# Kernel tuning notes

Hardware: AMD Instinct MI355X
Metric: run time of the kernel (lower is better)

## Reference

```python
import jax, jax.numpy as jnp
import numpy as np

B, T, D = 4, 2048, 1024

def setup_inputs() -> dict:
    key = jax.random.key(0)
    kx, kq, kk, kv = jax.random.split(key, 4)
    return {
        "vector": jax.random.normal(kx, (B, T, D), dtype=jnp.float32),
        # original uses torch.rand -> uniform [0,1)
        "W_queries": jax.random.uniform(kq, (D, D), dtype=jnp.float32),
        "W_keys": jax.random.uniform(kk, (D, D), dtype=jnp.float32),
        "W_values": jax.random.uniform(kv, (D, D), dtype=jnp.float32),
    }

def reference(vector, W_queries, W_keys, W_values):
    b, num_token, d_out = vector.shape
    queries = vector @ W_queries          # [b, t, d]
    keys = vector @ W_keys                # [b, t, d]
    values = vector @ W_values            # [b, t, d]
    # attention_score: [b, q, k]
    scores = jnp.einsum('bqd,bkd->bqk', queries, keys)
    causal_mask = jnp.triu(jnp.ones((num_token, num_token), dtype=bool), k=1)
    scores = jnp.where(causal_mask[None, :, :], -jnp.inf, scores)
    # NOTE: original uses FLOOR division `//` by sqrt(d_k) -- faithful here.
    inv_sqrt_scale = jnp.asarray(np.sqrt(keys.shape[-1]), dtype=scores.dtype)
    weights = jnp.floor(scores / inv_sqrt_scale)
    # NOTE: original applies softmax over dim=1 (the query axis), not dim=-1.
    weights = jax.nn.softmax(weights, axis=1)
    # dropout rate is 0.0 (eval/deterministic): identity
    context = jnp.einsum('bqk,bkd->bqd', weights, values)
    return context
```

## Files before the change

### kernel.cpp

```cpp
#include <hip/hip_runtime.h>
#include <math.h>

typedef _Float16 half4 __attribute__((ext_vector_type(4)));
typedef _Float16 half8 __attribute__((ext_vector_type(8)));
typedef float f32x4 __attribute__((ext_vector_type(4)));

#define GLD16(gptr, lptr)                                                     \
    __builtin_amdgcn_global_load_lds(                                         \
        (const __attribute__((address_space(1))) unsigned int*)(gptr),        \
        (__attribute__((address_space(3))) unsigned int*)(lptr), 16, 0, 0)

#define WAIT_VM(N) asm volatile("s_waitcnt vmcnt(" #N ")" ::: "memory")
#define WAIT_LGKM0() asm volatile("s_waitcnt lgkmcnt(0)" ::: "memory")
#define BARRIER()  __builtin_amdgcn_s_barrier()
#define SCHED_FENCE() __builtin_amdgcn_sched_barrier(0)

namespace {

constexpr int Bb = 4;
constexpr int Tt = 2048;
constexpr int Dd = 1024;
constexpr int BT = Bb * Tt;
constexpr int NCH = 16;

__device__ inline _Float16 f2h(float f) { return (_Float16)f; }

__global__ __launch_bounds__(256) void convert_all_kernel(
    const float* __restrict__ X,  const float* __restrict__ Wq,
    const float* __restrict__ Wk, const float* __restrict__ Wv,
    _Float16* __restrict__ Xhi, _Float16* __restrict__ Xlo,
    _Float16* __restrict__ Wqh, _Float16* __restrict__ Wql,
    _Float16* __restrict__ Wkh, _Float16* __restrict__ Wkl,
    _Float16* __restrict__ WvTh)
{
    __shared__ float tile[64][65];
    const int f = blockIdx.x;
    if (f < 8192) {
        const int idx = f * 1024 + threadIdx.x * 4;
        const float4 v = *(const float4*)(X + idx);
        const float a[4] = {v.x, v.y, v.z, v.w};
        half4 h, l;
#pragma unroll
        for (int i = 0; i < 4; ++i) {
            h[i] = f2h(a[i]);
            l[i] = f2h(a[i] - (float)h[i]);
        }
        *(half4*)(Xhi + idx) = h;
        *(half4*)(Xlo + idx) = l;
    } else if (f < 10240) {
        const int g = f - 8192;
        const int mat = g >> 10;
        const float* W = mat ? Wk : Wq;
        _Float16* Hh = mat ? Wkh : Wqh;
        _Float16* Ll = mat ? Wkl : Wql;
        const int idx = (g & 1023) * 1024 + threadIdx.x * 4;
        const float4 v = *(const float4*)(W + idx);
        const float a[4] = {v.x, v.y, v.z, v.w};
        half4 h, l;
#pragma unroll
        for (int i = 0; i < 4; ++i) {
            h[i] = f2h(a[i]);
            l[i] = f2h(a[i] - (float)h[i]);
        }
        *(half4*)(Hh + idx) = h;
        *(half4*)(Ll + idx) = l;
    } else {
        const int g = f - 10240;
        const int n0 = (g & 15) * 64, k0 = (g >> 4) * 64;
        const int tx = threadIdx.x & 63, ty = threadIdx.x >> 6;
#pragma unroll
        for (int i = 0; i < 16; ++i)
            tile[ty + i * 4][tx] = Wv[(size_t)(k0 + ty + i * 4) * Dd + n0 + tx];
        __syncthreads();
#pragma unroll
        for (int i = 0; i < 16; ++i) {
            const float v = tile[tx][ty + i * 4];
            WvTh[(size_t)(n0 + ty + i * 4) * Dd + k0 + tx] = f2h(v);
        }
    }
}

__global__ __launch_bounds__(256) void gt_kernel(
    const _Float16* __restrict__ Wkh, const _Float16* __restrict__ Wkl,
    const _Float16* __restrict__ Wqh, const _Float16* __restrict__ Wql,
    _Float16* __restrict__ GTh, _Float16* __restrict__ GTl)
{
    __shared__ _Float16 Ahl[2][2][4][512];
    __shared__ _Float16 Bhl[2][2][4][512];

    const int n0 = blockIdx.x * 64;
    const int m0 = blockIdx.y * 64;
    const int tid = threadIdx.x;
    const int w = tid >> 6, lane = tid & 63;
    const int lr = lane & 15, lq = lane >> 4;
    const int wi = (w >> 1) * 2, wj = (w & 1) * 2;

    f32x4 acc[2][2];
#pragma unroll
    for (int i = 0; i < 2; ++i)
#pragma unroll
        for (int j = 0; j < 2; ++j)
#pragma unroll
            for (int c = 0; c < 4; ++c) acc[i][j][c] = 0.f;

    auto stage = [&](int bf, int kk) {
        const int s = w;
        const size_t ar = (size_t)(m0 + s * 16 + lr) * Dd + kk + lq * 8;
        const size_t br = (size_t)(n0 + s * 16 + lr) * Dd + kk + lq * 8;
        GLD16(Wkh + ar, &Ahl[bf][0][s][0]);
        GLD16(Wkl + ar, &Ahl[bf][1][s][0]);
        GLD16(Wqh + br, &Bhl[bf][0][s][0]);
        GLD16(Wql + br, &Bhl[bf][1][s][0]);
    };

    stage(0, 0);
    int ib = 0;
    for (int step = 0; step < 32; ++step, ib ^= 1) {
        if (step < 31) {
            stage(ib ^ 1, (step + 1) << 5);
            WAIT_VM(4);
        } else {
            WAIT_VM(0);
        }
        BARRIER();
        SCHED_FENCE();
        half8 ah[2], al[2], bh[2], bl[2];
#pragma unroll
        for (int i = 0; i < 2; ++i) {
            ah[i] = *(const half8*)&Ahl[ib][0][wi + i][lane * 8];
            al[i] = *(const half8*)&Ahl[ib][1][wi + i][lane * 8];
        }
#pragma unroll
        for (int j = 0; j < 2; ++j) {
            bh[j] = *(const half8*)&Bhl[ib][0][wj + j][lane * 8];
            bl[j] = *(const half8*)&Bhl[ib][1][wj + j][lane * 8];
        }
#pragma unroll
        for (int i = 0; i < 2; ++i)
#pragma unroll
            for (int j = 0; j < 2; ++j) {
                acc[i][j] = __builtin_amdgcn_mfma_f32_16x16x32_f16(ah[i], bh[j], acc[i][j], 0, 0, 0);
                acc[i][j] = __builtin_amdgcn_mfma_f32_16x16x32_f16(ah[i], bl[j], acc[i][j], 0, 0, 0);
                acc[i][j] = __builtin_amdgcn_mfma_f32_16x16x32_f16(al[i], bh[j], acc[i][j], 0, 0, 0);
            }
        BARRIER();
    }

#pragma unroll
    for (int i = 0; i < 2; ++i)
#pragma unroll
        for (int r = 0; r < 4; ++r) {
            const int row = m0 + (wi + i) * 16 + lq * 4 + r;
#pragma unroll
            for (int j = 0; j < 2; ++j) {
                const int col = n0 + (wj + j) * 16 + lr;
                const float v = acc[i][j][r];
                const _Float16 h = f2h(v);
                GTh[(size_t)row * Dd + col] = h;
                GTl[(size_t)row * Dd + col] = f2h(v - (float)h);
            }
        }
}

__global__ __launch_bounds__(512, 4) void tv_kernel(
    const _Float16* __restrict__ Xhi, const _Float16* __restrict__ Xlo,
    const _Float16* __restrict__ GTh, const _Float16* __restrict__ GTl,
    const _Float16* __restrict__ WvTh,
    _Float16* __restrict__ Thi, _Float16* __restrict__ Tlo,
    _Float16* __restrict__ Vt)
{
    __shared__ _Float16 smem[32768];
    auto A_ = [&](int bf, int hl, int s) -> _Float16* {
        return smem + ((bf * 2 + hl) * 8 + s) * 512;
    };
    auto B_ = [&](int bf, int hl, int s) -> _Float16* {
        return smem + 16384 + ((bf * 2 + hl) * 8 + s) * 512;
    };

    const int f   = blockIdx.x;
    const int xcd = f & 7;
    const int c   = (f >> 3) & 31;
    const int p   = f >> 8;
    const int mb  = xcd * 8 + (c & 7);
    const int sub = p * 4 + (c >> 3);
    const int m0 = mb * 128;
    const int n0 = (sub & 7) * 128;

    const int tid = threadIdx.x;
    const int w = tid >> 6, lane = tid & 63;
    const int lr = lane & 15, lq = lane >> 4;
    const int wr = (w >> 1) * 2;
    const int wc = (w & 1) * 4;

    f32x4 acc[2][4];
#pragma unroll
    for (int i = 0; i < 2; ++i)
#pragma unroll
        for (int j = 0; j < 4; ++j)
#pragma unroll
            for (int c2 = 0; c2 < 4; ++c2) acc[i][j][c2] = 0.f;

    if (sub < 8) {
        auto stage = [&](int bf, int kk) {
            const size_t ar = (size_t)(m0 + w * 16 + lr) * Dd + kk + lq * 8;
            const size_t br = (size_t)(n0 + w * 16 + lr) * Dd + kk + lq * 8;
            GLD16(Xhi + ar, A_(bf, 0, w));
            GLD16(Xlo + ar, A_(bf, 1, w));
            GLD16(GTh + br, B_(bf, 0, w));
            GLD16(GTl + br, B_(bf, 1, w));
        };
        stage(0, 0);
        int ib = 0;
        for (int step = 0; step < 32; ++step, ib ^= 1) {
            if (step < 31) {
                stage(ib ^ 1, (step + 1) << 5);
                WAIT_VM(4);
            } else {
                WAIT_VM(0);
            }
            BARRIER();
            SCHED_FENCE();
            half8 ah[2], al[2], bh[4], bl[4];
#pragma unroll
            for (int i = 0; i < 2; ++i) {
                ah[i] = *(const half8*)(A_(ib, 0, wr + i) + lane * 8);
                al[i] = *(const half8*)(A_(ib, 1, wr + i) + lane * 8);
            }
#pragma unroll
            for (int j = 0; j < 4; ++j) {
                bh[j] = *(const half8*)(B_(ib, 0, wc + j) + lane * 8);
                bl[j] = *(const half8*)(B_(ib, 1, wc + j) + lane * 8);
            }
#pragma unroll
            for (int i = 0; i < 2; ++i)
#pragma unroll
                for (int j = 0; j < 4; ++j) {
                    acc[i][j] = __builtin_amdgcn_mfma_f32_16x16x32_f16(ah[i], bh[j], acc[i][j], 0, 0, 0);
                    acc[i][j] = __builtin_amdgcn_mfma_f32_16x16x32_f16(ah[i], bl[j], acc[i][j], 0, 0, 0);
                    acc[i][j] = __builtin_amdgcn_mfma_f32_16x16x32_f16(al[i], bh[j], acc[i][j], 0, 0, 0);
                }
            BARRIER();
        }
#pragma unroll
        for (int i = 0; i < 2; ++i)
#pragma unroll
            for (int r = 0; r < 4; ++r) {
                const int row = m0 + (wr + i) * 16 + lq * 4 + r;
#pragma unroll
                for (int j = 0; j < 4; ++j) {
                    const int col = n0 + (wc + j) * 16 + lr;
                    const float v = acc[i][j][r];
                    const _Float16 h = f2h(v);
                    Thi[(size_t)row * Dd + col] = h;
                    Tlo[(size_t)row * Dd + col] = f2h(v - (float)h);
                }
            }
    } else {
        auto stage = [&](int bf, int kk) {
            GLD16(Xhi + (size_t)(m0 + w * 16 + lr) * Dd + kk + lq * 8, A_(bf, 0, w));
            GLD16(WvTh + (size_t)(n0 + w * 16 + lr) * Dd + kk + lq * 8, B_(bf, 0, w));
        };
        stage(0, 0);
        int ib = 0;
        for (int step = 0; step < 32; ++step, ib ^= 1) {
            if (step < 31) {
                stage(ib ^ 1, (step + 1) << 5);
                WAIT_VM(2);
            } else {
                WAIT_VM(0);
            }
            BARRIER();
            SCHED_FENCE();
            half8 a[2], b2[4];
#pragma unroll
            for (int i = 0; i < 2; ++i) a[i] = *(const half8*)(A_(ib, 0, wr + i) + lane * 8);
#pragma unroll
            for (int j = 0; j < 4; ++j) b2[j] = *(const half8*)(B_(ib, 0, wc + j) + lane * 8);
#pragma unroll
            for (int i = 0; i < 2; ++i)
#pragma unroll
                for (int j = 0; j < 4; ++j)
                    acc[i][j] = __builtin_amdgcn_mfma_f32_16x16x32_f16(a[i], b2[j], acc[i][j], 0, 0, 0);
            BARRIER();
        }
        __syncthreads();
#pragma unroll
        for (int i = 0; i < 2; ++i)
#pragma unroll
            for (int r2 = 0; r2 < 4; ++r2) {
                const int rloc = (wr + i) * 16 + lq * 4 + r2;
#pragma unroll
                for (int j = 0; j < 4; ++j) {
                    const int cloc = (wc + j) * 16 + lr;
                    smem[cloc * 136 + rloc] = f2h(acc[i][j][r2]);
                }
            }
        __syncthreads();
        const int b2i = m0 >> 11;
        const int t0  = m0 & 2047;
        const int dloc = tid >> 2, tl = (tid & 3) * 32;
        _Float16* vp = Vt + (size_t)b2i * Dd * Tt + (size_t)(n0 + dloc) * Tt + t0 + tl;
#pragma unroll
        for (int e = 0; e < 4; ++e)
            *(half8*)(vp + e * 8) = *(const half8*)&smem[dloc * 136 + tl + e * 8];
    }
}

__global__ __launch_bounds__(512, 4) void scores_mfma_kernel(
    const _Float16* __restrict__ Thi, const _Float16* __restrict__ Tlo,
    const _Float16* __restrict__ Xhi, const _Float16* __restrict__ Xlo,
    _Float16* __restrict__ Pp, float* __restrict__ Pm, float* __restrict__ Pl)
{
    const int f  = blockIdx.x;
    const int fp = (f & 7) * 68 + (f >> 3);
    const int b = fp / 136;
    const int t = fp - b * 136;
    int byi = (int)((sqrtf(8.f * t + 1.f) - 1.f) * 0.5f);
    if ((byi + 1) * (byi + 2) / 2 <= t) ++byi;
    if (byi * (byi + 1) / 2 > t) --byi;
    const int bxi = t - byi * (byi + 1) / 2;
    const int j0 = bxi * 128, q0 = byi * 128;
    _Float16* Pb = Pp + (size_t)b * Tt * Tt;

    __shared__ _Float16 Ahl[2][2][8][512];
    __shared__ _Float16 Bhl[2][2][8][512];
    const _Float16* Th = Thi + (size_t)b * Tt * Dd;
    const _Float16* Tl = Tlo + (size_t)b * Tt * Dd;
    const _Float16* Xh = Xhi + (size_t)b * Tt * Dd;
    const _Float16* Xl = Xlo + (size_t)b * Tt * Dd;

    const int tid = threadIdx.x;
    const int w = tid >> 6, lane = tid & 63;
    const int lr = lane & 15, lq = lane >> 4;
    const int wr = (w >> 1) * 2;
    const int wc = (w & 1) * 4;

    f32x4 acc[2][4];
#pragma unroll
    for (int i = 0; i < 2; ++i)
#pragma unroll
        for (int j = 0; j < 4; ++j)
#pragma unroll
            for (int c = 0; c < 4; ++c) acc[i][j][c] = 0.f;

    auto stage = [&](int bf, int kk) {
        const size_t ar = (size_t)(q0 + w * 16 + lr) * Dd + kk + lq * 8;
        const size_t br = (size_t)(j0 + w * 16 + lr) * Dd + kk + lq * 8;
        GLD16(Th + ar, &Ahl[bf][0][w][0]);
        GLD16(Tl + ar, &Ahl[bf][1][w][0]);
        GLD16(Xh + br, &Bhl[bf][0][w][0]);
        GLD16(Xl + br, &Bhl[bf][1][w][0]);
    };

    stage(0, 0);
    int ib = 0;
    for (int step = 0; step < 32; ++step, ib ^= 1) {
        if (step < 31) {
            stage(ib ^ 1, (step + 1) << 5);
            WAIT_VM(4);
        } else {
            WAIT_VM(0);
        }
        BARRIER();
        SCHED_FENCE();
        half8 ah[2], al[2], bh[4], bl[4];
#pragma unroll
        for (int i = 0; i < 2; ++i) {
            ah[i] = *(const half8*)&Ahl[ib][0][wr + i][lane * 8];
            al[i] = *(const half8*)&Ahl[ib][1][wr + i][lane * 8];
        }
#pragma unroll
        for (int j = 0; j < 4; ++j) {
            bh[j] = *(const half8*)&Bhl[ib][0][wc + j][lane * 8];
            bl[j] = *(const half8*)&Bhl[ib][1][wc + j][lane * 8];
        }
#pragma unroll
        for (int i = 0; i < 2; ++i)
#pragma unroll
            for (int j = 0; j < 4; ++j) {
                acc[i][j] = __builtin_amdgcn_mfma_f32_16x16x32_f16(ah[i], bh[j], acc[i][j], 0, 0, 0);
                acc[i][j] = __builtin_amdgcn_mfma_f32_16x16x32_f16(ah[i], bl[j], acc[i][j], 0, 0, 0);
                acc[i][j] = __builtin_amdgcn_mfma_f32_16x16x32_f16(al[i], bh[j], acc[i][j], 0, 0, 0);
            }
        BARRIER();
    }

    float sv[2][4][4];
#pragma unroll
    for (int i = 0; i < 2; ++i)
#pragma unroll
        for (int r = 0; r < 4; ++r) {
            const int q = q0 + (wr + i) * 16 + lq * 4 + r;
#pragma unroll
            for (int j = 0; j < 4; ++j) {
                const int jg = j0 + (wc + j) * 16 + lr;
                sv[i][j][r] = (jg <= q) ? floorf(acc[i][j][r] * 0.03125f) : -INFINITY;
            }
        }

    float* red  = (float*)&Ahl[0][0][0][0];
    float* colm = red + 4096;
    __syncthreads();
    for (int e = tid; e < 4096; e += 512) red[e] = -INFINITY;
    __syncthreads();
    const int rowidx = (w * 4 + lq) * 128;
#pragma unroll
    for (int j = 0; j < 4; ++j) {
        const int c = (wc + j) * 16 + lr;
        float lm = -INFINITY;
#pragma unroll
        for (int i = 0; i < 2; ++i)
#pragma unroll
            for (int r = 0; r < 4; ++r) lm = fmaxf(lm, sv[i][j][r]);
        red[rowidx + c] = lm;
    }
    __syncthreads();
    if (tid < 128) {
        float m = -INFINITY;
#pragma unroll
        for (int e = 0; e < 32; ++e) m = fmaxf(m, red[e * 128 + tid]);
        colm[tid] = m;
    }
    __syncthreads();
    float ls[4];
#pragma unroll
    for (int j = 0; j < 4; ++j) {
        const int c = (wc + j) * 16 + lr;
        const int jg = j0 + c;
        const float m = colm[c];
        float s = 0.f;
#pragma unroll
        for (int i = 0; i < 2; ++i)
#pragma unroll
            for (int r = 0; r < 4; ++r) {
                const float e = __expf(sv[i][j][r] - m);
                s += e;
                const int q = q0 + (wr + i) * 16 + lq * 4 + r;
                Pb[(size_t)q * Tt + jg] = f2h(e);
            }
        ls[j] = s;
    }
    __syncthreads();
    for (int e = tid; e < 4096; e += 512) red[e] = 0.f;
    __syncthreads();
#pragma unroll
    for (int j = 0; j < 4; ++j) red[rowidx + (wc + j) * 16 + lr] = ls[j];
    __syncthreads();
    if (tid < 128) {
        float l = 0.f;
#pragma unroll
        for (int e = 0; e < 32; ++e) l += red[e * 128 + tid];
        const size_t o = ((size_t)b * NCH + byi) * Tt + j0 + tid;
        Pm[o] = colm[tid];
        Pl[o] = l;
    }
}

__global__ __launch_bounds__(256) void colstats_merge_kernel(
    const float* __restrict__ Pm, const float* __restrict__ Pl,
    float* __restrict__ Mb, float* __restrict__ Lb)
{
    const int j = blockIdx.x * 256 + threadIdx.x;
    const int b = blockIdx.y;
    const int jt = j >> 7;
    float m = -INFINITY, l = 0.f;
    for (int c = jt; c < NCH; ++c) {
        const size_t pidx = ((size_t)b * NCH + c) * Tt + j;
        const float mi = Pm[pidx];
        if (mi == -INFINITY) continue;
        const float li = Pl[pidx];
        if (mi > m) { l = l * __expf(m - mi) + li; m = mi; }
        else        { l += li * __expf(mi - m); }
    }
    Mb[(size_t)b * Tt + j] = m;
    Lb[(size_t)b * Tt + j] = (l > 0.f) ? 1.f / l : 0.f;
}

__global__ __launch_bounds__(256) void context_mfma_kernel(
    const _Float16* __restrict__ Pp, const float* __restrict__ Pm,
    const float* __restrict__ Mb, const float* __restrict__ Lb,
    const _Float16* __restrict__ Vt, float* __restrict__ Out)
{
    __shared__ _Float16 As[2][8][512];
    __shared__ _Float16 Bl[2][8][512];
    __shared__ float cbuf[2048];

    const int f   = blockIdx.x;
    const int xcd = f & 7;
    const int c   = (f >> 3) & 31;
    const int p   = f >> 8;
    const int b   = xcd >> 1;
    const int bx  = c & 7;
    const int base = ((xcd & 1) << 3) + ((c >> 3) << 1);
    const int by  = p ? (15 - base) : base;
    const int d0 = bx * 128;
    const int q0 = by * 128;
    const _Float16* Pb = Pp + (size_t)b * Tt * Tt;
    const float* Pmb = Pm + ((size_t)b * NCH + by) * Tt;
    const float* Mp = Mb + (size_t)b * Tt;
    const float* Lp = Lb + (size_t)b * Tt;
    const _Float16* Vb = Vt + (size_t)b * Dd * Tt;
    float* Ob = Out + (size_t)b * Tt * Dd;

    const int tid = threadIdx.x;
    const int w = tid >> 6, lane = tid & 63;
    const int lr = lane & 15, lq = lane >> 4;
    const int wr = (w >> 1) * 4, wc = (w & 1) * 4;
    const int kmax = q0 + 128;
    const int nstep = kmax >> 5;

    for (int k = tid; k < kmax; k += 256)
        cbuf[k] = __expf(Pmb[k] - Mp[k]) * Lp[k];

    f32x4 acc[4][4];
#pragma unroll
    for (int i = 0; i < 4; ++i)
#pragma unroll
        for (int j = 0; j < 4; ++j)
#pragma unroll
            for (int c2 = 0; c2 < 4; ++c2) acc[i][j][c2] = 0.f;

    half8 RpA[2], RpB[2];
    auto loadP = [&](half8 (&R)[2], int k0) {
#pragma unroll
        for (int s2 = 0; s2 < 2; ++s2) {
            const int s = w * 2 + s2;
            R[s2] = *(const half8*)(Pb + (size_t)(q0 + s * 16 + lr) * Tt + k0 + lq * 8);
        }
    };
    auto issueV = [&](int bf, int k0) {
#pragma unroll
        for (int s2 = 0; s2 < 2; ++s2) {
            const int s = w * 2 + s2;
            GLD16(Vb + (size_t)(d0 + s * 16 + lr) * Tt + k0 + lq * 8, &Bl[bf][s][0]);
        }
    };
    auto writeA = [&](int bf, half8 (&R)[2], int k0) {
        const float* cp = cbuf + k0 + lq * 8;
        float cv[8];
#pragma unroll
        for (int e = 0; e < 8; ++e) cv[e] = cp[e];
#pragma unroll
        for (int s2 = 0; s2 < 2; ++s2) {
            const int s = w * 2 + s2;
            half8 out;
#pragma unroll
            for (int e = 0; e < 8; ++e) out[e] = f2h((float)R[s2][e] * cv[e]);
            *(half8*)&As[bf][s][lane * 8] = out;
        }
    };
    auto domfma = [&](int bf) {
        half8 a[4], b2[4];
#pragma unroll
        for (int i = 0; i < 4; ++i) a[i] = *(const half8*)&As[bf][wr + i][lane * 8];
#pragma unroll
        for (int j = 0; j < 4; ++j) b2[j] = *(const half8*)&Bl[bf][wc + j][lane * 8];
#pragma unroll
        for (int i = 0; i < 4; ++i)
#pragma unroll
            for (int j = 0; j < 4; ++j)
                acc[i][j] = __builtin_amdgcn_mfma_f32_16x16x32_f16(a[i], b2[j], acc[i][j], 0, 0, 0);
    };

    __syncthreads();

    issueV(0, 0);
    loadP(RpA, 0);
    loadP(RpB, 32);
    WAIT_VM(2);
    writeA(0, RpA, 0);
    WAIT_LGKM0();
    BARRIER();

    for (int i = 0; i < nstep; i += 2) {
        {
            const bool pfP = (i + 2 < nstep);
            issueV(1, (i + 1) << 5);
            if (pfP) loadP(RpA, (i + 2) << 5);
            domfma(0);
            if (pfP) WAIT_VM(4); else WAIT_VM(2);
            writeA(1, RpB, (i + 1) << 5);
            if (pfP) WAIT_VM(2); else WAIT_VM(0);
            WAIT_LGKM0();
            BARRIER();
        }
        {
            const bool pfV = (i + 2 < nstep);
            const bool pfP = (i + 3 < nstep);
            if (pfV) issueV(0, (i + 2) << 5);
            if (pfP) loadP(RpB, (i + 3) << 5);
            domfma(1);
            if (pfV) {
                if (pfP) WAIT_VM(4); else WAIT_VM(2);
                writeA(0, RpA, (i + 2) << 5);
                if (pfP) WAIT_VM(2); else WAIT_VM(0);
                WAIT_LGKM0();
            }
            BARRIER();
        }
    }

#pragma unroll
    for (int i = 0; i < 4; ++i)
#pragma unroll
        for (int r2 = 0; r2 < 4; ++r2) {
            const int row = q0 + (wr + i) * 16 + lq * 4 + r2;
#pragma unroll
            for (int j = 0; j < 4; ++j)
                Ob[(size_t)row * Dd + d0 + (wc + j) * 16 + lr] = acc[i][j][r2];
        }
}

}

extern "C" void kernel_launch(void* const* d_in, const int* in_sizes, int n_in,
                              void* d_out, int out_size, void* d_ws, size_t ws_size,
                              hipStream_t stream)
{
    const float* X  = (const float*)d_in[0];
    const float* Wq = (const float*)d_in[1];
    const float* Wk = (const float*)d_in[2];
    const float* Wv = (const float*)d_in[3];

    char* ws = (char*)d_ws;
    const size_t MB = 1024 * 1024;
    _Float16* Xhi  = (_Float16*)ws;
    _Float16* Xlo  = (_Float16*)(ws + 16 * MB);
    _Float16* Wqh  = (_Float16*)(ws + 32 * MB);
    _Float16* Wql  = (_Float16*)(ws + 34 * MB);
    _Float16* Wkh  = (_Float16*)(ws + 36 * MB);
    _Float16* Wkl  = (_Float16*)(ws + 38 * MB);
    _Float16* WvTh = (_Float16*)(ws + 40 * MB);
    _Float16* GTh  = (_Float16*)(ws + 44 * MB);
    _Float16* GTl  = (_Float16*)(ws + 46 * MB);
    _Float16* Thi  = (_Float16*)(ws + 48 * MB);
    _Float16* Tlo  = (_Float16*)(ws + 64 * MB);
    _Float16* Vt   = (_Float16*)(ws + 80 * MB);
    _Float16* Pp   = (_Float16*)(ws + 112 * MB);
    float*    Mb   = (float*)(ws + 176 * MB);
    float*    Lb   = Mb + (size_t)Bb * Tt;
    float*    Pm   = Lb + (size_t)Bb * Tt;
    float*    Pl   = Pm + (size_t)Bb * NCH * Tt;
    float*    Out  = (float*)d_out;

    convert_all_kernel<<<10496, 256, 0, stream>>>(X, Wq, Wk, Wv, Xhi, Xlo,
                                                  Wqh, Wql, Wkh, Wkl, WvTh);
    gt_kernel<<<dim3(16, 16), 256, 0, stream>>>(Wkh, Wkl, Wqh, Wql, GTh, GTl);
    tv_kernel<<<dim3(1024), 512, 0, stream>>>(Xhi, Xlo, GTh, GTl, WvTh, Thi, Tlo, Vt);
    scores_mfma_kernel<<<dim3(544), 512, 0, stream>>>(Thi, Tlo, Xhi, Xlo, Pp, Pm, Pl);
    colstats_merge_kernel<<<dim3(Tt / 256, Bb), 256, 0, stream>>>(Pm, Pl, Mb, Lb);
    context_mfma_kernel<<<dim3(512), 256, 0, stream>>>(Pp, Pm, Mb, Lb, Vt, Out);
}
```

Before: 389.3 us.

## Single-buffer scores kernel LDS staging and raise occupancy bound

```diff
diff --git a/kernel.cpp b/kernel.cpp
--- a/kernel.cpp
+++ b/kernel.cpp
@@ -306,7 +306,7 @@
     }
 }
 
-__global__ __launch_bounds__(512, 4) void scores_mfma_kernel(
+__global__ __launch_bounds__(512, 8) void scores_mfma_kernel(
     const _Float16* __restrict__ Thi, const _Float16* __restrict__ Tlo,
     const _Float16* __restrict__ Xhi, const _Float16* __restrict__ Xlo,
     _Float16* __restrict__ Pp, float* __restrict__ Pm, float* __restrict__ Pl)
@@ -322,8 +322,8 @@
     const int j0 = bxi * 128, q0 = byi * 128;
     _Float16* Pb = Pp + (size_t)b * Tt * Tt;
 
-    __shared__ _Float16 Ahl[2][2][8][512];
-    __shared__ _Float16 Bhl[2][2][8][512];
+    __shared__ _Float16 Ahl[2][8][512];
+    __shared__ _Float16 Bhl[2][8][512];
     const _Float16* Th = Thi + (size_t)b * Tt * Dd;
     const _Float16* Tl = Tlo + (size_t)b * Tt * Dd;
     const _Float16* Xh = Xhi + (size_t)b * Tt * Dd;
@@ -343,36 +343,29 @@
 #pragma unroll
             for (int c = 0; c < 4; ++c) acc[i][j][c] = 0.f;
 
-    auto stage = [&](int bf, int kk) {
-        const size_t ar = (size_t)(q0 + w * 16 + lr) * Dd + kk + lq * 8;
-        const size_t br = (size_t)(j0 + w * 16 + lr) * Dd + kk + lq * 8;
-        GLD16(Th + ar, &Ahl[bf][0][w][0]);
-        GLD16(Tl + ar, &Ahl[bf][1][w][0]);
-        GLD16(Xh + br, &Bhl[bf][0][w][0]);
-        GLD16(Xl + br, &Bhl[bf][1][w][0]);
-    };
-
-    stage(0, 0);
-    int ib = 0;
-    for (int step = 0; step < 32; ++step, ib ^= 1) {
-        if (step < 31) {
-            stage(ib ^ 1, (step + 1) << 5);
-            WAIT_VM(4);
-        } else {
-            WAIT_VM(0);
-        }
+    const size_t ar0 = (size_t)(q0 + w * 16 + lr) * Dd + lq * 8;
+    const size_t br0 = (size_t)(j0 + w * 16 + lr) * Dd + lq * 8;
+
+    for (int step = 0; step < 32; ++step) {
+        const int kk = step << 5;
+        BARRIER();
+        GLD16(Th + ar0 + kk, &Ahl[0][w][0]);
+        GLD16(Tl + ar0 + kk, &Ahl[1][w][0]);
+        GLD16(Xh + br0 + kk, &Bhl[0][w][0]);
+        GLD16(Xl + br0 + kk, &Bhl[1][w][0]);
+        WAIT_VM(0);
         BARRIER();
         SCHED_FENCE();
         half8 ah[2], al[2], bh[4], bl[4];
 #pragma unroll
         for (int i = 0; i < 2; ++i) {
-            ah[i] = *(const half8*)&Ahl[ib][0][wr + i][lane * 8];
-            al[i] = *(const half8*)&Ahl[ib][1][wr + i][lane * 8];
+            ah[i] = *(const half8*)&Ahl[0][wr + i][lane * 8];
+            al[i] = *(const half8*)&Ahl[1][wr + i][lane * 8];
         }
 #pragma unroll
         for (int j = 0; j < 4; ++j) {
-            bh[j] = *(const half8*)&Bhl[ib][0][wc + j][lane * 8];
-            bl[j] = *(const half8*)&Bhl[ib][1][wc + j][lane * 8];
+            bh[j] = *(const half8*)&Bhl[0][wc + j][lane * 8];
+            bl[j] = *(const half8*)&Bhl[1][wc + j][lane * 8];
         }
 #pragma unroll
         for (int i = 0; i < 2; ++i)
@@ -382,7 +375,6 @@
                 acc[i][j] = __builtin_amdgcn_mfma_f32_16x16x32_f16(ah[i], bl[j], acc[i][j], 0, 0, 0);
                 acc[i][j] = __builtin_amdgcn_mfma_f32_16x16x32_f16(al[i], bh[j], acc[i][j], 0, 0, 0);
             }
-        BARRIER();
     }
 
     float sv[2][4][4];
@@ -398,8 +390,8 @@
             }
         }
 
-    float* red  = (float*)&Ahl[0][0][0][0];
-    float* colm = red + 4096;
+    float* red  = (float*)&Ahl[0][0][0];
+    float* colm = (float*)&Bhl[0][0][0];
     __syncthreads();
     for (int e = tid; e < 4096; e += 512) red[e] = -INFINITY;
     __syncthreads();
```

After: 569.5 us. 46.3% more time.
